# Kernel optimization log

Measured on AMD Instinct MI355X. Metric: run time of the kernel, lower is better.

Reference implementation:

```python
import jax, jax.numpy as jnp
import numpy as np

NUM_LAYERS = 20   # num_layers init arg
RPRIME = 1.0      # Rprime init arg
HIDDEN = 512      # hidden_size
G, P = 64, 16     # num polygons, polygon size (graph.structure)
N, D = 65536, 2   # points, input_size


def _simplex_project(x):
    """KDS.activate: sort-based Euclidean projection onto the probability simplex, rows of x."""
    n = x.shape[-1]
    u = -jnp.sort(-x, axis=-1)                                   # descending sort
    v = (jnp.cumsum(u, axis=-1) - 1.0) / jnp.arange(1, n + 1, dtype=x.dtype)
    k = jnp.sum(u > v, axis=-1) - 1                               # rho - 1 (always >= 0)
    w = jnp.take_along_axis(v, k[..., None], axis=-1)             # threshold tau per row
    return jax.nn.relu(x - w)


def _nesterov_coeff(layer):
    return layer / (layer + 3.0)


def _poca(y, A, step):
    """point_of_closest_approach: accelerated projected GD onto conv hull of A's rows.
    y: [N, D], A: [P, D] -> [N, D]"""
    n = y.shape[0]
    p = A.shape[0]
    init = (jnp.zeros((n, p), y.dtype), jnp.zeros((n, p), y.dtype))  # (x_tmp, x_old)

    def body(carry, layer):
        x_tmp, x_old = carry
        Q = jnp.nan_to_num(y - x_tmp @ A)          # [N, D]
        grad = -(Q @ A.T)                          # [N, P]
        x_new = _simplex_project(x_tmp - grad * step)
        x_tmp_next = x_new + _nesterov_coeff(layer) * (x_new - x_old)
        return (x_tmp_next, x_new), None

    (_, x_new), _ = jax.lax.scan(body, init, jnp.arange(NUM_LAYERS, dtype=y.dtype))
    return x_new @ A                               # [N, D]


def setup_inputs() -> dict:
    key = jax.random.key(0)
    k1, k2, k3, k4 = jax.random.split(key, 4)
    y = jax.random.normal(k1, (N, D), dtype=jnp.float32)
    W = jax.random.normal(k2, (HIDDEN, D), dtype=jnp.float32)
    step = jax.random.uniform(k3, (1,), dtype=jnp.float32)
    polygons = jax.random.randint(k4, (G, P), 0, HIDDEN, dtype=jnp.int32)
    return {"y": y, "W": W, "step": step, "polygons": polygons}


def reference(y, W, step, polygons):
    """KDS.forward with accelerate=True == encode_accelerated(y).
    Returns (yhat, f, f0) matching the torch module's encode output."""
    step_s = step[0]
    A = W[polygons]                                               # [G, P, D] gather
    points = jax.vmap(lambda a: _poca(y, a, step_s))(A)           # [G, N, D]

    # gradient is constant across outer iterations: [N, G+1]
    dist = jnp.sqrt(jnp.sum((y[None, :, :] - points) ** 2, axis=-1) / (RPRIME ** 2))  # [G, N]
    grad = jnp.concatenate([jnp.ones((y.shape[0], 1), y.dtype), dist.T], axis=1)

    init = (jnp.zeros((y.shape[0], G + 1), y.dtype),
            jnp.zeros((y.shape[0], G + 1), y.dtype))              # (f_tmp, f_old)

    def body(carry, layer):
        f_tmp, f_old = carry
        f_new = _simplex_project(f_tmp - grad * step_s)
        f_tmp_next = f_new + _nesterov_coeff(layer) * (f_new - f_old)
        return (f_tmp_next, f_new), None

    (_, f_new), _ = jax.lax.scan(body, init, jnp.arange(NUM_LAYERS, dtype=y.dtype))

    yhat = y * f_new[:, :1] + jnp.einsum('ng,gnd->nd', f_new[:, 1:], points)
    return yhat, f_new[:, 1:], f_new[:, 0]
```

## Files before the change

### kernel.cpp

```cpp
#include <hip/hip_runtime.h>
#include <math.h>

#define NPTS  65536
#define NG    64
#define NP    16
#define NLAY  20

__global__ __launch_bounds__(256) void poca_kernel(
    const float* __restrict__ y, const float* __restrict__ W,
    const float* __restrict__ step_p, const int* __restrict__ polys,
    float2* __restrict__ pts)
{
    const int g = blockIdx.y;
    const int n = blockIdx.x * 256 + threadIdx.x;
    const float step = step_p[0];

    float a0[NP], a1[NP];
#pragma unroll
    for (int p = 0; p < NP; ++p) {
        const int idx = polys[g * NP + p];
        a0[p] = W[idx * 2 + 0];
        a1[p] = W[idx * 2 + 1];
    }

    const float y0 = y[2 * n + 0];
    const float y1 = y[2 * n + 1];

    float xt[NP], xo[NP];
#pragma unroll
    for (int p = 0; p < NP; ++p) { xt[p] = 0.f; xo[p] = 0.f; }

    for (int layer = 0; layer < NLAY; ++layer) {
        float q0 = y0, q1 = y1;
#pragma unroll
        for (int p = 0; p < NP; ++p) {
            q0 = fmaf(-xt[p], a0[p], q0);
            q1 = fmaf(-xt[p], a1[p], q1);
        }
        float x[NP], u[NP];
#pragma unroll
        for (int p = 0; p < NP; ++p) {
            const float d = fmaf(q0, a0[p], q1 * a1[p]);
            x[p] = fmaf(step, d, xt[p]);
            u[p] = x[p];
        }
#pragma unroll
        for (int k = 2; k <= NP; k <<= 1) {
#pragma unroll
            for (int j = k >> 1; j > 0; j >>= 1) {
#pragma unroll
                for (int i = 0; i < NP; ++i) {
                    const int l = i ^ j;
                    if (l > i) {
                        const bool up = ((i & k) == 0);
                        const float mx = fmaxf(u[i], u[l]);
                        const float mn = fminf(u[i], u[l]);
                        u[i] = up ? mx : mn;
                        u[l] = up ? mn : mx;
                    }
                }
            }
        }
        float cs = u[0];
        float tau = cs - 1.0f;
#pragma unroll
        for (int j = 1; j < NP; ++j) {
            cs += u[j];
            const float vv = (cs - 1.0f) * (1.0f / (float)(j + 1));
            tau = (u[j] > vv) ? vv : tau;
        }
        const float c = (float)layer / ((float)layer + 3.0f);
#pragma unroll
        for (int p = 0; p < NP; ++p) {
            const float xn = fmaxf(x[p] - tau, 0.f);
            xt[p] = fmaf(c, xn - xo[p], xn);
            xo[p] = xn;
        }
    }

    float p0 = 0.f, p1 = 0.f;
#pragma unroll
    for (int p = 0; p < NP; ++p) {
        p0 = fmaf(xo[p], a0[p], p0);
        p1 = fmaf(xo[p], a1[p], p1);
    }
    pts[(size_t)g * NPTS + n] = make_float2(p0, p1);
}

__global__ __launch_bounds__(256) void fiter_kernel(
    const float* __restrict__ y, const float* __restrict__ step_p,
    const float2* __restrict__ pts, float* __restrict__ out)
{
    const int n = blockIdx.x * 256 + threadIdx.x;
    const float step = step_p[0];
    const float y0 = y[2 * n + 0];
    const float y1 = y[2 * n + 1];

    float gs[NG + 1];
    gs[0] = step;
#pragma unroll
    for (int g = 0; g < NG; ++g) {
        const float2 p = pts[(size_t)g * NPTS + n];
        const float dx = y0 - p.x;
        const float dy = y1 - p.y;
        gs[1 + g] = sqrtf(dx * dx + dy * dy) * step;
    }

    float x[NG + 1], fo[NG + 1];
#pragma unroll
    for (int i = 0; i <= NG; ++i) { x[i] = 0.f; fo[i] = 0.f; }

    for (int layer = 0; layer < NLAY; ++layer) {
        float s0 = 0.f, s1 = 0.f, s2 = 0.f, s3 = 0.f;
#pragma unroll
        for (int i = 0; i <= NG; ++i) {
            x[i] -= gs[i];
            if ((i & 3) == 0)      s0 += x[i];
            else if ((i & 3) == 1) s1 += x[i];
            else if ((i & 3) == 2) s2 += x[i];
            else                   s3 += x[i];
        }
        float tau = ((s0 + s1) + (s2 + s3) - 1.0f) * (1.0f / 65.0f);
        int kprev = NG + 1;
        for (int pass = 0; pass < NG + 1; ++pass) {
            float t0 = 0.f, t1 = 0.f, t2 = 0.f, t3 = 0.f;
            int cnt = 0;
#pragma unroll
            for (int i = 0; i <= NG; ++i) {
                const bool in = x[i] > tau;
                const float xv = in ? x[i] : 0.f;
                if ((i & 3) == 0)      t0 += xv;
                else if ((i & 3) == 1) t1 += xv;
                else if ((i & 3) == 2) t2 += xv;
                else                   t3 += xv;
                cnt += in ? 1 : 0;
            }
            if (cnt == kprev) break;
            kprev = cnt;
            tau = (((t0 + t1) + (t2 + t3)) - 1.0f) / (float)cnt;
        }
        const float c = (float)layer / ((float)layer + 3.0f);
#pragma unroll
        for (int i = 0; i <= NG; ++i) {
            const float fn = fmaxf(x[i] - tau, 0.f);
            x[i] = fmaf(c, fn - fo[i], fn);
            fo[i] = fn;
        }
    }

    float acc0 = y0 * fo[0];
    float acc1 = y1 * fo[0];
#pragma unroll
    for (int g = 0; g < NG; ++g) {
        const float2 p = pts[(size_t)g * NPTS + n];
        acc0 = fmaf(fo[1 + g], p.x, acc0);
        acc1 = fmaf(fo[1 + g], p.y, acc1);
    }

    ((float2*)out)[n] = make_float2(acc0, acc1);
    float4* fsec = (float4*)(out + 2 * (size_t)NPTS);
#pragma unroll
    for (int g4 = 0; g4 < NG / 4; ++g4) {
        fsec[(size_t)n * (NG / 4) + g4] = make_float4(
            fo[1 + 4 * g4], fo[2 + 4 * g4], fo[3 + 4 * g4], fo[4 + 4 * g4]);
    }
    out[2 * (size_t)NPTS + (size_t)NPTS * NG + n] = fo[0];
}

extern "C" void kernel_launch(void* const* d_in, const int* in_sizes, int n_in,
                              void* d_out, int out_size, void* d_ws, size_t ws_size,
                              hipStream_t stream) {
    const float* y      = (const float*)d_in[0];
    const float* W      = (const float*)d_in[1];
    const float* step   = (const float*)d_in[2];
    const int*   polys  = (const int*)d_in[3];
    float*       out    = (float*)d_out;
    float2*      pts    = (float2*)d_ws;

    dim3 gridA(NPTS / 256, NG);
    poca_kernel<<<gridA, 256, 0, stream>>>(y, W, step, polys, pts);
    fiter_kernel<<<NPTS / 256, 256, 0, stream>>>(y, step, pts, out);
}
```

Measured before the change: 731.7 us.

## Process two points per thread in poca kernel using packed float2 math

Each thread of the polygon projection kernel now handles two points at once, using 2-wide float vectors so the compiler can emit packed FP32 instructions (v_pk_fma/max/min). The step factor is folded into the polygon vertices ahead of time, and the threshold selection in the simplex projection becomes a running max instead of a compare-select. Loads and stores become float4. This halves the thread count and doubles register pressure per thread, which may reduce occupancy.

```diff
diff --git a/kernel.cpp b/kernel.cpp
--- a/kernel.cpp
+++ b/kernel.cpp
@@ -6,42 +6,49 @@
 #define NP    16
 #define NLAY  20
 
+typedef float f32x2 __attribute__((ext_vector_type(2)));
+
+__device__ __forceinline__ f32x2 splat(float s) { f32x2 r; r.x = s; r.y = s; return r; }
+
 __global__ __launch_bounds__(256) void poca_kernel(
-    const float* __restrict__ y, const float* __restrict__ W,
+    const float4* __restrict__ y4, const float* __restrict__ W,
     const float* __restrict__ step_p, const int* __restrict__ polys,
-    float2* __restrict__ pts)
+    float4* __restrict__ pts4)
 {
     const int g = blockIdx.y;
-    const int n = blockIdx.x * 256 + threadIdx.x;
+    const int t = blockIdx.x * 256 + threadIdx.x;
     const float step = step_p[0];
 
-    float a0[NP], a1[NP];
+    float a0[NP], a1[NP], sa0[NP], sa1[NP];
 #pragma unroll
     for (int p = 0; p < NP; ++p) {
         const int idx = polys[g * NP + p];
         a0[p] = W[idx * 2 + 0];
         a1[p] = W[idx * 2 + 1];
+        sa0[p] = step * a0[p];
+        sa1[p] = step * a1[p];
     }
 
-    const float y0 = y[2 * n + 0];
-    const float y1 = y[2 * n + 1];
+    const float4 yv = y4[t];
+    const f32x2 y0 = { yv.x, yv.z };
+    const f32x2 y1 = { yv.y, yv.w };
 
-    float xt[NP], xo[NP];
+    f32x2 xt[NP], xo[NP];
 #pragma unroll
-    for (int p = 0; p < NP; ++p) { xt[p] = 0.f; xo[p] = 0.f; }
+    for (int p = 0; p < NP; ++p) { xt[p] = splat(0.f); xo[p] = splat(0.f); }
 
     for (int layer = 0; layer < NLAY; ++layer) {
-        float q0 = y0, q1 = y1;
+        f32x2 q0 = y0, q1 = y1;
 #pragma unroll
         for (int p = 0; p < NP; ++p) {
-            q0 = fmaf(-xt[p], a0[p], q0);
-            q1 = fmaf(-xt[p], a1[p], q1);
+            q0 -= xt[p] * splat(a0[p]);
+            q1 -= xt[p] * splat(a1[p]);
         }
-        float x[NP], u[NP];
+        f32x2 x[NP], u[NP];
 #pragma unroll
         for (int p = 0; p < NP; ++p) {
-            const float d = fmaf(q0, a0[p], q1 * a1[p]);
-            x[p] = fmaf(step, d, xt[p]);
+            x[p] = __builtin_elementwise_fma(q0, splat(sa0[p]),
+                   __builtin_elementwise_fma(q1, splat(sa1[p]), xt[p]));
             u[p] = x[p];
         }
 #pragma unroll
@@ -53,38 +60,39 @@
                     const int l = i ^ j;
                     if (l > i) {
                         const bool up = ((i & k) == 0);
-                        const float mx = fmaxf(u[i], u[l]);
-                        const float mn = fminf(u[i], u[l]);
+                        const f32x2 mx = __builtin_elementwise_max(u[i], u[l]);
+                        const f32x2 mn = __builtin_elementwise_min(u[i], u[l]);
                         u[i] = up ? mx : mn;
                         u[l] = up ? mn : mx;
                     }
                 }
             }
         }
-        float cs = u[0];
-        float tau = cs - 1.0f;
+        f32x2 cs  = u[0];
+        f32x2 tau = cs - splat(1.0f);
 #pragma unroll
         for (int j = 1; j < NP; ++j) {
             cs += u[j];
-            const float vv = (cs - 1.0f) * (1.0f / (float)(j + 1));
-            tau = (u[j] > vv) ? vv : tau;
+            const float c = 1.0f / (float)(j + 1);
+            const f32x2 vj = __builtin_elementwise_fma(cs, splat(c), splat(-c));
+            tau = __builtin_elementwise_max(tau, vj);
         }
-        const float c = (float)layer / ((float)layer + 3.0f);
+        const float cn = (float)layer / ((float)layer + 3.0f);
 #pragma unroll
         for (int p = 0; p < NP; ++p) {
-            const float xn = fmaxf(x[p] - tau, 0.f);
-            xt[p] = fmaf(c, xn - xo[p], xn);
+            const f32x2 xn = __builtin_elementwise_max(x[p] - tau, splat(0.f));
+            xt[p] = __builtin_elementwise_fma(splat(cn), xn - xo[p], xn);
             xo[p] = xn;
         }
     }
 
-    float p0 = 0.f, p1 = 0.f;
+    f32x2 p0 = splat(0.f), p1 = splat(0.f);
 #pragma unroll
     for (int p = 0; p < NP; ++p) {
-        p0 = fmaf(xo[p], a0[p], p0);
-        p1 = fmaf(xo[p], a1[p], p1);
+        p0 = __builtin_elementwise_fma(xo[p], splat(a0[p]), p0);
+        p1 = __builtin_elementwise_fma(xo[p], splat(a1[p]), p1);
     }
-    pts[(size_t)g * NPTS + n] = make_float2(p0, p1);
+    pts4[(size_t)g * (NPTS / 2) + t] = make_float4(p0.x, p1.x, p0.y, p1.y);
 }
 
 __global__ __launch_bounds__(256) void fiter_kernel(
@@ -170,14 +178,16 @@
 extern "C" void kernel_launch(void* const* d_in, const int* in_sizes, int n_in,
                               void* d_out, int out_size, void* d_ws, size_t ws_size,
                               hipStream_t stream) {
-    const float* y      = (const float*)d_in[0];
-    const float* W      = (const float*)d_in[1];
-    const float* step   = (const float*)d_in[2];
-    const int*   polys  = (const int*)d_in[3];
-    float*       out    = (float*)d_out;
-    float2*      pts    = (float2*)d_ws;
+    const float*  y     = (const float*)d_in[0];
+    const float4* y4    = (const float4*)d_in[0];
+    const float*  W     = (const float*)d_in[1];
+    const float*  step  = (const float*)d_in[2];
+    const int*    polys = (const int*)d_in[3];
+    float*        out   = (float*)d_out;
+    float4*       pts4  = (float4*)d_ws;
+    const float2* pts2  = (const float2*)d_ws;
 
-    dim3 gridA(NPTS / 256, NG);
-    poca_kernel<<<gridA, 256, 0, stream>>>(y, W, step, polys, pts);
-    fiter_kernel<<<NPTS / 256, 256, 0, stream>>>(y, step, pts, out);
+    dim3 gridA(NPTS / 2 / 256, NG);
+    poca_kernel<<<gridA, 256, 0, stream>>>(y4, W, step, polys, pts4);
+    fiter_kernel<<<NPTS / 256, 256, 0, stream>>>(y, step, pts2, out);
 }
```

Result: no change. 740.2 us (+1.2%).
